# Kernel tuning notes

Hardware: AMD Instinct MI355X
Metric: run time of the kernel (lower is better)

Reference implementation:

```python
import jax, jax.numpy as jnp
import numpy as np

LAMBD = 0.4  # hardshrink threshold used in effective_weight


def ternarize(W):
    # sign(hardshrink(W, 0.4)) -> values in {-1, 0, 1}
    return jnp.sign(jnp.where(jnp.abs(W) > LAMBD, W, 0.0))


def setup_inputs() -> dict:
    key = jax.random.key(0)
    k1, k2 = jax.random.split(key)
    x = jax.random.normal(k1, (8192, 2048), dtype=jnp.float32)
    W = jax.random.normal(k2, (8192, 2048), dtype=jnp.float32)  # [n_out, n_in]
    return {"x": x, "W": W}


def reference(x, W):
    # discretize_weight() copies effective (ternary) weight into linear.weight,
    # then forward is a plain bias-free linear: y = x @ W_eff.T
    W_eff = ternarize(W)
    return jnp.einsum("ti,oi->to", x, W_eff)
```

## Files before the change

### kernel.cpp

```cpp
#include <hip/hip_runtime.h>
#include <stdint.h>

typedef __attribute__((ext_vector_type(4))) int i32x4;

#define M_DIM 8192
#define N_DIM 8192
#define K_DIM 2048
#define BK 128
#define NT (K_DIM / BK)

__global__ __launch_bounds__(256)
void tl_quant(const float* __restrict__ x, const float* __restrict__ W,
              signed char* __restrict__ xq, signed char* __restrict__ wq,
              float* __restrict__ srow) {
  __shared__ float smax[4];
  const int row = blockIdx.x;
  const int t = threadIdx.x;

  const float* xr = x + (size_t)row * K_DIM;
  float4 v0 = reinterpret_cast<const float4*>(xr)[t * 2];
  float4 v1 = reinterpret_cast<const float4*>(xr)[t * 2 + 1];
  float m = fmaxf(fmaxf(fmaxf(fabsf(v0.x), fabsf(v0.y)), fmaxf(fabsf(v0.z), fabsf(v0.w))),
                  fmaxf(fmaxf(fabsf(v1.x), fabsf(v1.y)), fmaxf(fabsf(v1.z), fabsf(v1.w))));
  #pragma unroll
  for (int off = 1; off < 64; off <<= 1)
    m = fmaxf(m, __shfl_xor(m, off, 64));
  if ((t & 63) == 0) smax[t >> 6] = m;
  __syncthreads();
  m = fmaxf(fmaxf(smax[0], smax[1]), fmaxf(smax[2], smax[3]));
  const float rs = (m > 0.f) ? 127.0f / m : 0.f;

  union { signed char c[8]; uint2 u; } qx;
  qx.c[0] = (signed char)__float2int_rn(v0.x * rs);
  qx.c[1] = (signed char)__float2int_rn(v0.y * rs);
  qx.c[2] = (signed char)__float2int_rn(v0.z * rs);
  qx.c[3] = (signed char)__float2int_rn(v0.w * rs);
  qx.c[4] = (signed char)__float2int_rn(v1.x * rs);
  qx.c[5] = (signed char)__float2int_rn(v1.y * rs);
  qx.c[6] = (signed char)__float2int_rn(v1.z * rs);
  qx.c[7] = (signed char)__float2int_rn(v1.w * rs);
  reinterpret_cast<uint2*>(xq + (size_t)row * K_DIM)[t] = qx.u;

  const float* wr = W + (size_t)row * K_DIM;
  float4 w0 = reinterpret_cast<const float4*>(wr)[t * 2];
  float4 w1 = reinterpret_cast<const float4*>(wr)[t * 2 + 1];
  union { signed char c[8]; uint2 u; } qw;
  qw.c[0] = (fabsf(w0.x) > 0.4f) ? ((w0.x > 0.f) ? 1 : -1) : 0;
  qw.c[1] = (fabsf(w0.y) > 0.4f) ? ((w0.y > 0.f) ? 1 : -1) : 0;
  qw.c[2] = (fabsf(w0.z) > 0.4f) ? ((w0.z > 0.f) ? 1 : -1) : 0;
  qw.c[3] = (fabsf(w0.w) > 0.4f) ? ((w0.w > 0.f) ? 1 : -1) : 0;
  qw.c[4] = (fabsf(w1.x) > 0.4f) ? ((w1.x > 0.f) ? 1 : -1) : 0;
  qw.c[5] = (fabsf(w1.y) > 0.4f) ? ((w1.y > 0.f) ? 1 : -1) : 0;
  qw.c[6] = (fabsf(w1.z) > 0.4f) ? ((w1.z > 0.f) ? 1 : -1) : 0;
  qw.c[7] = (fabsf(w1.w) > 0.4f) ? ((w1.w > 0.f) ? 1 : -1) : 0;
  reinterpret_cast<uint2*>(wq + (size_t)row * K_DIM)[t] = qw.u;

  if (t == 0) srow[row] = (m > 0.f) ? m / 127.0f : 0.f;
}

__global__ __launch_bounds__(256, 4)
void tl_gemm(const signed char* __restrict__ A, const signed char* __restrict__ B,
             const float* __restrict__ srow, float* __restrict__ C) {
  __shared__ signed char sA[128 * 128];
  __shared__ signed char sB[128 * 128];

  const int tid  = threadIdx.x;
  const int lane = tid & 63;
  const int w    = tid >> 6;
  const int wr   = w >> 1;
  const int wc   = w & 1;

  const int bid = blockIdx.x;
  const int xcd = bid & 7;
  const int idx = bid >> 3;
  const int s   = idx >> 6;
  const int t   = idx & 63;
  const int tm  = xcd * 8 + (t & 7);
  const int tn  = s * 8 + (t >> 3);
  const size_t brow = (size_t)tm * 128;
  const size_t bcol = (size_t)tn * 128;

  const int srow0  = w * 32 + (lane >> 3);
  const int scolb0 = (lane & 7) * 16;

  i32x4 acc[4][4];
  #pragma unroll
  for (int i = 0; i < 4; ++i)
    #pragma unroll
    for (int j = 0; j < 4; ++j)
      acc[i][j] = i32x4{0, 0, 0, 0};

  const int fr = lane & 15;
  const int k8 = lane >> 4;

  for (int kt = 0; kt < K_DIM; kt += BK) {
    #pragma unroll
    for (int j = 0; j < 4; ++j) {
      int row  = srow0 + j * 8;
      int colb = scolb0 ^ ((row & 7) << 4);
      const signed char* ga = A + (brow + row) * (size_t)K_DIM + kt + colb;
      const signed char* gb = B + (bcol + row) * (size_t)K_DIM + kt + colb;
      signed char* la = &sA[(w * 32 + j * 8) * 128];
      signed char* lb = &sB[(w * 32 + j * 8) * 128];
      __builtin_amdgcn_global_load_lds((const __attribute__((address_space(1))) void*)ga,
                                       (__attribute__((address_space(3))) void*)la, 16, 0, 0);
      __builtin_amdgcn_global_load_lds((const __attribute__((address_space(1))) void*)gb,
                                       (__attribute__((address_space(3))) void*)lb, 16, 0, 0);
    }
    __syncthreads();

    #pragma unroll
    for (int kk = 0; kk < 2; ++kk) {
      i32x4 av[4], bv[4];
      #pragma unroll
      for (int mi = 0; mi < 4; ++mi) {
        int row  = wr * 64 + mi * 16 + fr;
        int colb = (kk * 64 + k8 * 16) ^ ((row & 7) << 4);
        av[mi] = *(const i32x4*)&sA[row * 128 + colb];
      }
      #pragma unroll
      for (int ni = 0; ni < 4; ++ni) {
        int row  = wc * 64 + ni * 16 + fr;
        int colb = (kk * 64 + k8 * 16) ^ ((row & 7) << 4);
        bv[ni] = *(const i32x4*)&sB[row * 128 + colb];
      }
      #pragma unroll
      for (int mi = 0; mi < 4; ++mi)
        #pragma unroll
        for (int ni = 0; ni < 4; ++ni)
          acc[mi][ni] = __builtin_amdgcn_mfma_i32_16x16x64_i8(av[mi], bv[ni], acc[mi][ni], 0, 0, 0);
    }
    __syncthreads();
  }

  #pragma unroll
  for (int mi = 0; mi < 4; ++mi) {
    size_t r0 = brow + wr * 64 + mi * 16 + k8 * 4;
    float sc0 = srow[r0 + 0], sc1 = srow[r0 + 1], sc2 = srow[r0 + 2], sc3 = srow[r0 + 3];
    #pragma unroll
    for (int ni = 0; ni < 4; ++ni) {
      i32x4 v = acc[mi][ni];
      size_t c0 = bcol + wc * 64 + ni * 16 + fr;
      C[(r0 + 0) * N_DIM + c0] = sc0 * (float)v[0];
      C[(r0 + 1) * N_DIM + c0] = sc1 * (float)v[1];
      C[(r0 + 2) * N_DIM + c0] = sc2 * (float)v[2];
      C[(r0 + 3) * N_DIM + c0] = sc3 * (float)v[3];
    }
  }
}

__global__ void tl_naive(const float* __restrict__ x, const float* __restrict__ W,
                         float* __restrict__ out) {
  __shared__ float sx[16][17];
  __shared__ float sw[16][17];
  int tx = threadIdx.x, ty = threadIdx.y;
  int row = blockIdx.y * 16 + ty;
  int col = blockIdx.x * 16 + tx;
  float acc = 0.f;
  for (int kt = 0; kt < K_DIM; kt += 16) {
    sx[ty][tx] = x[(size_t)row * K_DIM + kt + tx];
    float wv = W[(size_t)(blockIdx.x * 16 + ty) * K_DIM + kt + tx];
    sw[ty][tx] = (fabsf(wv) > 0.4f) ? ((wv > 0.f) ? 1.f : -1.f) : 0.f;
    __syncthreads();
    #pragma unroll
    for (int k = 0; k < 16; ++k) acc += sx[ty][k] * sw[tx][k];
    __syncthreads();
  }
  out[(size_t)row * N_DIM + col] = acc;
}

extern "C" void kernel_launch(void* const* d_in, const int* in_sizes, int n_in,
                              void* d_out, int out_size, void* d_ws, size_t ws_size,
                              hipStream_t stream) {
  const float* x = (const float*)d_in[0];
  const float* W = (const float*)d_in[1];
  float* out = (float*)d_out;

  const size_t xq_bytes = (size_t)M_DIM * K_DIM;
  const size_t wq_bytes = (size_t)N_DIM * K_DIM;
  const size_t need = xq_bytes + wq_bytes + M_DIM * sizeof(float);

  if (ws_size >= need) {
    signed char* xq = (signed char*)d_ws;
    signed char* wq = xq + xq_bytes;
    float* srow = (float*)(wq + wq_bytes);
    tl_quant<<<M_DIM, 256, 0, stream>>>(x, W, xq, wq, srow);
    tl_gemm<<<4096, 256, 0, stream>>>(xq, wq, srow, out);
  } else {
    dim3 g(N_DIM / 16, M_DIM / 16), b(16, 16);
    tl_naive<<<g, b, 0, stream>>>(x, W, out);
  }
}
```

Before: 185.7 us.

## Pre-swizzle quantized activations into MFMA fragment layout and load A directly from global

```diff
diff --git a/kernel.cpp b/kernel.cpp
--- a/kernel.cpp
+++ b/kernel.cpp
@@ -8,6 +8,7 @@
 #define K_DIM 2048
 #define BK 128
 #define NT (K_DIM / BK)
+#define K64 (K_DIM / 64)
 
 __global__ __launch_bounds__(256)
 void tl_quant(const float* __restrict__ x, const float* __restrict__ W,
@@ -39,7 +40,12 @@
   qx.c[5] = (signed char)__float2int_rn(v1.y * rs);
   qx.c[6] = (signed char)__float2int_rn(v1.z * rs);
   qx.c[7] = (signed char)__float2int_rn(v1.w * rs);
-  reinterpret_cast<uint2*>(xq + (size_t)row * K_DIM)[t] = qx.u;
+  {
+    const int m16 = row >> 4, fr = row & 15;
+    const int k64 = t >> 3, k8 = (t >> 1) & 3, b8 = t & 1;
+    const size_t u2 = (((size_t)m16 * K64 + k64) * 64 + (k8 * 16 + fr)) * 2 + b8;
+    reinterpret_cast<uint2*>(xq)[u2] = qx.u;
+  }
 
   const float* wr = W + (size_t)row * K_DIM;
   float4 w0 = reinterpret_cast<const float4*>(wr)[t * 2];
@@ -59,9 +65,8 @@
 }
 
 __global__ __launch_bounds__(256, 4)
-void tl_gemm(const signed char* __restrict__ A, const signed char* __restrict__ B,
+void tl_gemm(const signed char* __restrict__ Af, const signed char* __restrict__ B,
              const float* __restrict__ srow, float* __restrict__ C) {
-  __shared__ signed char sA[128 * 128];
   __shared__ signed char sB[128 * 128];
 
   const int tid  = threadIdx.x;
@@ -93,42 +98,61 @@
   const int fr = lane & 15;
   const int k8 = lane >> 4;
 
+  const int m16g = tm * 8 + wr * 4;
+  const size_t laneoff = (size_t)lane * 16;
+
   for (int kt = 0; kt < K_DIM; kt += BK) {
+    const int k64 = kt >> 6;
+
     #pragma unroll
     for (int j = 0; j < 4; ++j) {
       int row  = srow0 + j * 8;
       int colb = scolb0 ^ ((row & 7) << 4);
-      const signed char* ga = A + (brow + row) * (size_t)K_DIM + kt + colb;
       const signed char* gb = B + (bcol + row) * (size_t)K_DIM + kt + colb;
-      signed char* la = &sA[(w * 32 + j * 8) * 128];
       signed char* lb = &sB[(w * 32 + j * 8) * 128];
-      __builtin_amdgcn_global_load_lds((const __attribute__((address_space(1))) void*)ga,
-                                       (__attribute__((address_space(3))) void*)la, 16, 0, 0);
       __builtin_amdgcn_global_load_lds((const __attribute__((address_space(1))) void*)gb,
                                        (__attribute__((address_space(3))) void*)lb, 16, 0, 0);
     }
-    __syncthreads();
-
-    #pragma unroll
-    for (int kk = 0; kk < 2; ++kk) {
-      i32x4 av[4], bv[4];
-      #pragma unroll
-      for (int mi = 0; mi < 4; ++mi) {
-        int row  = wr * 64 + mi * 16 + fr;
-        int colb = (kk * 64 + k8 * 16) ^ ((row & 7) << 4);
-        av[mi] = *(const i32x4*)&sA[row * 128 + colb];
-      }
+
+    i32x4 av0[4];
+    #pragma unroll
+    for (int mi = 0; mi < 4; ++mi)
+      av0[mi] = *(const i32x4*)(Af + (((size_t)(m16g + mi) * K64 + k64) << 10) + laneoff);
+
+    __syncthreads();
+
+    i32x4 av1[4];
+    #pragma unroll
+    for (int mi = 0; mi < 4; ++mi)
+      av1[mi] = *(const i32x4*)(Af + (((size_t)(m16g + mi) * K64 + k64 + 1) << 10) + laneoff);
+
+    {
+      i32x4 bv[4];
       #pragma unroll
       for (int ni = 0; ni < 4; ++ni) {
         int row  = wc * 64 + ni * 16 + fr;
-        int colb = (kk * 64 + k8 * 16) ^ ((row & 7) << 4);
+        int colb = (k8 * 16) ^ ((row & 7) << 4);
         bv[ni] = *(const i32x4*)&sB[row * 128 + colb];
       }
       #pragma unroll
       for (int mi = 0; mi < 4; ++mi)
         #pragma unroll
         for (int ni = 0; ni < 4; ++ni)
-          acc[mi][ni] = __builtin_amdgcn_mfma_i32_16x16x64_i8(av[mi], bv[ni], acc[mi][ni], 0, 0, 0);
+          acc[mi][ni] = __builtin_amdgcn_mfma_i32_16x16x64_i8(av0[mi], bv[ni], acc[mi][ni], 0, 0, 0);
+    }
+    {
+      i32x4 bv[4];
+      #pragma unroll
+      for (int ni = 0; ni < 4; ++ni) {
+        int row  = wc * 64 + ni * 16 + fr;
+        int colb = (64 + k8 * 16) ^ ((row & 7) << 4);
+        bv[ni] = *(const i32x4*)&sB[row * 128 + colb];
+      }
+      #pragma unroll
+      for (int mi = 0; mi < 4; ++mi)
+        #pragma unroll
+        for (int ni = 0; ni < 4; ++ni)
+          acc[mi][ni] = __builtin_amdgcn_mfma_i32_16x16x64_i8(av1[mi], bv[ni], acc[mi][ni], 0, 0, 0);
     }
     __syncthreads();
   }
```

Result: slower. 200.9 us (+8.2%).
